# Optimization experiments

Hardware: AMD Instinct MI355X
Metric: run time of the kernel (lower is better)

Reference implementation:

```python
import jax, jax.numpy as jnp
import numpy as np

B, D, H = 64, 1024, 1024  # batch, input_dim, hidden_dim


def setup_inputs() -> dict:
    key = jax.random.key(0)
    k_x, k_inW, k_hW = jax.random.split(key, 3)
    # Observed binary inputs in {0,1} -> Bernoulli-sample branch never taken.
    x = jax.random.randint(k_x, (B, D), 0, 2).astype(jnp.float32)
    # Kaiming-normal init: std = sqrt(2 / fan_in)
    in_W = jax.random.normal(k_inW, (H, D), dtype=jnp.float32) * np.float32(np.sqrt(2.0 / D))
    in_b = jnp.zeros((H,), dtype=jnp.float32)
    h_W = jax.random.normal(k_hW, (D, H), dtype=jnp.float32) * np.float32(np.sqrt(2.0 / H))
    h_b = jnp.zeros((D,), dtype=jnp.float32)
    return {"x": x, "in_W": in_W, "in_b": in_b, "h_W": h_W, "h_b": h_b}


def reference(x, in_W, in_b, h_W, h_b):
    # NADE recurrence: a_i = in_b + sum_{j<i} x_j * in_W[:, j]
    # Vectorized via exclusive cumulative sum of rank-1 contributions.
    contrib = jnp.einsum("bd,hd->bdh", x, in_W)          # [B, D, H]
    cum = jnp.cumsum(contrib, axis=1)
    a = jnp.concatenate([jnp.zeros_like(cum[:, :1]), cum[:, :-1]], axis=1) + in_b  # exclusive
    h = jax.nn.relu(a)                                    # [B, D, H]
    # p_i = sigmoid(relu(a_i) . h_W[i] + h_b[i])
    p_hat = jax.nn.sigmoid(jnp.einsum("bdh,dh->bd", h, h_W) + h_b)  # [B, D]
    return p_hat
```

## Files before the change

### kernel.cpp

```cpp
#include <hip/hip_runtime.h>
#include <hip/hip_bf16.h>

#define B 64
#define D 1024
#define H 1024
#define C 32
#define L (D / C)

__device__ __forceinline__ float dpp_xor1(float v) {
    int i = __builtin_bit_cast(int, v);
    i = __builtin_amdgcn_mov_dpp(i, 0xB1, 0xF, 0xF, true);
    return __builtin_bit_cast(float, i);
}
__device__ __forceinline__ float dpp_xor2(float v) {
    int i = __builtin_bit_cast(int, v);
    i = __builtin_amdgcn_mov_dpp(i, 0x4E, 0xF, 0xF, true);
    return __builtin_bit_cast(float, i);
}

__global__ void k_transpose(const float* __restrict__ in, float* __restrict__ out) {
    __shared__ float tile[32][33];
    int bx = blockIdx.x * 32;
    int by = blockIdx.y * 32;
    int tx = threadIdx.x;
    int ty = threadIdx.y;
    #pragma unroll
    for (int r = 0; r < 32; r += 8)
        tile[ty + r][tx] = in[(by + ty + r) * D + (bx + tx)];
    __syncthreads();
    #pragma unroll
    for (int r = 0; r < 32; r += 8)
        out[(bx + ty + r) * H + (by + tx)] = tile[tx][ty + r];
}

__global__ void __launch_bounds__(256, 4)
k_chunk_sums(const float* __restrict__ x,
             const float* __restrict__ Wt,
             float* __restrict__ S) {
    int blk = blockIdx.x;
    int b = blk / C;
    int c = blk % C;
    int tid = threadIdx.x;
    int h0 = tid * 4;

    __shared__ unsigned mlds;
    float xv = (tid < L) ? x[b * D + c * L + tid] : 0.f;
    unsigned long long bal = __ballot(xv != 0.f);
    if (tid == 0) mlds = (unsigned)bal;
    __syncthreads();
    unsigned m = mlds;

    float4 acc = make_float4(0.f, 0.f, 0.f, 0.f);
    #pragma unroll
    for (int j = 0; j < L; ++j) {
        if (m & (1u << j)) {
            float4 w = *reinterpret_cast<const float4*>(&Wt[(size_t)(c * L + j) * H + h0]);
            acc.x += w.x; acc.y += w.y; acc.z += w.z; acc.w += w.w;
        }
    }
    *reinterpret_cast<float4*>(&S[((size_t)b * C + c) * H + h0]) = acc;
}

__global__ void k_scan(float* __restrict__ S) {
    int tid = blockIdx.x * blockDim.x + threadIdx.x;
    if (tid >= B * H) return;
    int b = tid / H;
    int h = tid % H;
    float run = 0.f;
    #pragma unroll
    for (int c = 0; c < C; ++c) {
        int idx = (b * C + c) * H + h;
        float v = S[idx];
        S[idx] = run;
        run += v;
    }
}

__global__ void __launch_bounds__(256, 4)
k_nade_main(const float* __restrict__ x,
            const float* __restrict__ Wt,
            const float* __restrict__ in_b,
            const float* __restrict__ h_W,
            const float* __restrict__ h_b,
            const float* __restrict__ P,
            float* __restrict__ out) {
    int blk = blockIdx.x;
    int b = blk / C;
    int c = blk % C;
    int tid = threadIdx.x;
    int h0 = tid * 4;
    int lane = tid & 63;
    int wv = tid >> 6;
    int ph = lane & 3;

    __shared__ unsigned mlds;
    float xv = (tid < L) ? x[b * D + c * L + tid] : 0.f;
    unsigned long long bal = __ballot(xv != 0.f);
    if (tid == 0) mlds = (unsigned)bal;

    float4 pv = *reinterpret_cast<const float4*>(&P[((size_t)b * C + c) * H + h0]);
    float4 ib = *reinterpret_cast<const float4*>(&in_b[h0]);
    float4 a;
    a.x = pv.x + ib.x; a.y = pv.y + ib.y; a.z = pv.z + ib.z; a.w = pv.w + ib.w;

    __syncthreads();
    unsigned m = mlds;

    float pr[8];
    #pragma unroll
    for (int s = 0; s < 8; ++s) pr[s] = 0.f;

    #pragma unroll
    for (int il = 0; il < L; ++il) {
        int i = c * L + il;
        float4 w = *reinterpret_cast<const float4*>(&h_W[(size_t)i * H + h0]);
        float p = fmaxf(a.x, 0.f) * w.x + fmaxf(a.y, 0.f) * w.y +
                  fmaxf(a.z, 0.f) * w.z + fmaxf(a.w, 0.f) * w.w;
        float t = p + dpp_xor1(p);
        t = t + dpp_xor2(t);
        pr[il >> 2] = (ph == (il & 3)) ? t : pr[il >> 2];

        if (m & (1u << il)) {
            float4 wv4 = *reinterpret_cast<const float4*>(&Wt[(size_t)i * H + h0]);
            a.x += wv4.x; a.y += wv4.y; a.z += wv4.z; a.w += wv4.w;
        }
    }

    #pragma unroll
    for (int s = 0; s < 8; ++s) {
        float v = pr[s];
        v += __shfl_xor(v, 4, 64);
        v += __shfl_xor(v, 8, 64);
        v += __shfl_xor(v, 16, 64);
        v += __shfl_xor(v, 32, 64);
        pr[s] = v;
    }

    __shared__ float red[4][L];
    if (lane < 4) {
        #pragma unroll
        for (int s = 0; s < 8; ++s)
            red[wv][s * 4 + lane] = pr[s];
    }
    __syncthreads();

    if (tid < L) {
        int i = c * L + tid;
        float t = red[0][tid] + red[1][tid] + red[2][tid] + red[3][tid] + h_b[i];
        out[(size_t)b * D + i] = 1.0f / (1.0f + expf(-t));
    }
}

extern "C" void kernel_launch(void* const* d_in, const int* in_sizes, int n_in,
                              void* d_out, int out_size, void* d_ws, size_t ws_size,
                              hipStream_t stream) {
    const float* x    = (const float*)d_in[0];
    const float* in_W = (const float*)d_in[1];
    const float* in_b = (const float*)d_in[2];
    const float* h_W  = (const float*)d_in[3];
    const float* h_b  = (const float*)d_in[4];
    float* out = (float*)d_out;

    float* Wt = (float*)d_ws;
    float* S  = Wt + (size_t)D * H;

    dim3 tb(32, 8);
    dim3 tg(D / 32, H / 32);
    k_transpose<<<tg, tb, 0, stream>>>(in_W, Wt);

    k_chunk_sums<<<B * C, 256, 0, stream>>>(x, Wt, S);

    k_scan<<<(B * H + 255) / 256, 256, 0, stream>>>(S);

    k_nade_main<<<B * C, 256, 0, stream>>>(x, Wt, in_b, h_W, h_b, S, out);
}
```

Before: 45.57 us.

## Batch four rows per block and split hidden dim into quarters with combine pass

Each block now handles four batch rows and a quarter of the hidden dimension, so each loaded weight element (Wt and h_W) is reused across four batch rows instead of one. The sparse bitmask skip of zero inputs is replaced by dense FMAs with x values staged in shared memory. Partial dot products per hidden quarter go to a new workspace buffer Q, and a new combine kernel sums them and applies the sigmoid. This cuts weight traffic by about 4x. The costs are an extra launch, extra global traffic for Q, more registers, and losing the skip over zero inputs.

```diff
diff --git a/kernel.cpp b/kernel.cpp
--- a/kernel.cpp
+++ b/kernel.cpp
@@ -6,6 +6,10 @@
 #define H 1024
 #define C 32
 #define L (D / C)
+#define BG 4
+#define NBG (B / BG)
+#define HQ 4
+#define HP (H / HQ)
 
 __device__ __forceinline__ float dpp_xor1(float v) {
     int i = __builtin_bit_cast(int, v);
@@ -33,32 +37,43 @@
         out[(bx + ty + r) * H + (by + tx)] = tile[tx][ty + r];
 }
 
-__global__ void __launch_bounds__(256, 4)
+__global__ void __launch_bounds__(256)
 k_chunk_sums(const float* __restrict__ x,
              const float* __restrict__ Wt,
              float* __restrict__ S) {
     int blk = blockIdx.x;
-    int b = blk / C;
-    int c = blk % C;
+    int bg  = blk >> 7;
+    int chq = blk & 127;
+    int c   = chq >> 2;
+    int hq  = chq & 3;
+    int b0  = bg * BG;
     int tid = threadIdx.x;
-    int h0 = tid * 4;
-
-    __shared__ unsigned mlds;
-    float xv = (tid < L) ? x[b * D + c * L + tid] : 0.f;
-    unsigned long long bal = __ballot(xv != 0.f);
-    if (tid == 0) mlds = (unsigned)bal;
-    __syncthreads();
-    unsigned m = mlds;
-
-    float4 acc = make_float4(0.f, 0.f, 0.f, 0.f);
+    int h   = hq * HP + tid;
+
+    __shared__ float4 xs4[L];
+    if (tid < L) {
+        int i = c * L + tid;
+        xs4[tid] = make_float4(x[(size_t)b0 * D + i],
+                               x[(size_t)(b0 + 1) * D + i],
+                               x[(size_t)(b0 + 2) * D + i],
+                               x[(size_t)(b0 + 3) * D + i]);
+    }
+    __syncthreads();
+
+    float acc0 = 0.f, acc1 = 0.f, acc2 = 0.f, acc3 = 0.f;
     #pragma unroll
     for (int j = 0; j < L; ++j) {
-        if (m & (1u << j)) {
-            float4 w = *reinterpret_cast<const float4*>(&Wt[(size_t)(c * L + j) * H + h0]);
-            acc.x += w.x; acc.y += w.y; acc.z += w.z; acc.w += w.w;
-        }
-    }
-    *reinterpret_cast<float4*>(&S[((size_t)b * C + c) * H + h0]) = acc;
+        float w = Wt[(size_t)(c * L + j) * H + h];
+        float4 xf = xs4[j];
+        acc0 = fmaf(xf.x, w, acc0);
+        acc1 = fmaf(xf.y, w, acc1);
+        acc2 = fmaf(xf.z, w, acc2);
+        acc3 = fmaf(xf.w, w, acc3);
+    }
+    S[((size_t)b0 * C + c) * H + h]       = acc0;
+    S[((size_t)(b0 + 1) * C + c) * H + h] = acc1;
+    S[((size_t)(b0 + 2) * C + c) * H + h] = acc2;
+    S[((size_t)(b0 + 3) * C + c) * H + h] = acc3;
 }
 
 __global__ void k_scan(float* __restrict__ S) {
@@ -76,79 +91,130 @@
     }
 }
 
-__global__ void __launch_bounds__(256, 4)
+__global__ void __launch_bounds__(256)
 k_nade_main(const float* __restrict__ x,
             const float* __restrict__ Wt,
             const float* __restrict__ in_b,
             const float* __restrict__ h_W,
             const float* __restrict__ h_b,
             const float* __restrict__ P,
-            float* __restrict__ out) {
+            float* __restrict__ Q) {
     int blk = blockIdx.x;
-    int b = blk / C;
-    int c = blk % C;
+    int bg  = blk >> 7;
+    int chq = blk & 127;
+    int c   = chq >> 2;
+    int hq  = chq & 3;
+    int b0  = bg * BG;
     int tid = threadIdx.x;
-    int h0 = tid * 4;
+    int h   = hq * HP + tid;
     int lane = tid & 63;
     int wv = tid >> 6;
     int ph = lane & 3;
 
-    __shared__ unsigned mlds;
-    float xv = (tid < L) ? x[b * D + c * L + tid] : 0.f;
-    unsigned long long bal = __ballot(xv != 0.f);
-    if (tid == 0) mlds = (unsigned)bal;
-
-    float4 pv = *reinterpret_cast<const float4*>(&P[((size_t)b * C + c) * H + h0]);
-    float4 ib = *reinterpret_cast<const float4*>(&in_b[h0]);
-    float4 a;
-    a.x = pv.x + ib.x; a.y = pv.y + ib.y; a.z = pv.z + ib.z; a.w = pv.w + ib.w;
-
-    __syncthreads();
-    unsigned m = mlds;
-
-    float pr[8];
-    #pragma unroll
-    for (int s = 0; s < 8; ++s) pr[s] = 0.f;
+    __shared__ float4 xs4[L];
+    if (tid < L) {
+        int i = c * L + tid;
+        xs4[tid] = make_float4(x[(size_t)b0 * D + i],
+                               x[(size_t)(b0 + 1) * D + i],
+                               x[(size_t)(b0 + 2) * D + i],
+                               x[(size_t)(b0 + 3) * D + i]);
+    }
+
+    float ib = in_b[h];
+    float a0 = P[((size_t)b0 * C + c) * H + h] + ib;
+    float a1 = P[((size_t)(b0 + 1) * C + c) * H + h] + ib;
+    float a2 = P[((size_t)(b0 + 2) * C + c) * H + h] + ib;
+    float a3 = P[((size_t)(b0 + 3) * C + c) * H + h] + ib;
+
+    __syncthreads();
+
+    bool k0 = (ph == 0), k1 = (ph == 1), k2 = (ph == 2), k3 = (ph == 3);
+
+    float pr0[8], pr1[8], pr2[8], pr3[8];
+    #pragma unroll
+    for (int s = 0; s < 8; ++s) { pr0[s] = 0.f; pr1[s] = 0.f; pr2[s] = 0.f; pr3[s] = 0.f; }
 
     #pragma unroll
     for (int il = 0; il < L; ++il) {
         int i = c * L + il;
-        float4 w = *reinterpret_cast<const float4*>(&h_W[(size_t)i * H + h0]);
-        float p = fmaxf(a.x, 0.f) * w.x + fmaxf(a.y, 0.f) * w.y +
-                  fmaxf(a.z, 0.f) * w.z + fmaxf(a.w, 0.f) * w.w;
-        float t = p + dpp_xor1(p);
-        t = t + dpp_xor2(t);
-        pr[il >> 2] = (ph == (il & 3)) ? t : pr[il >> 2];
-
-        if (m & (1u << il)) {
-            float4 wv4 = *reinterpret_cast<const float4*>(&Wt[(size_t)i * H + h0]);
-            a.x += wv4.x; a.y += wv4.y; a.z += wv4.z; a.w += wv4.w;
-        }
+        float w  = h_W[(size_t)i * H + h];
+        float wt = Wt[(size_t)i * H + h];
+        float4 xf = xs4[il];
+        int s = il >> 2;
+        bool keep = (il & 3) == 0 ? k0 : ((il & 3) == 1 ? k1 : ((il & 3) == 2 ? k2 : k3));
+
+        float p0 = fmaxf(a0, 0.f) * w;
+        float t0 = p0 + dpp_xor1(p0); t0 = t0 + dpp_xor2(t0);
+        pr0[s] = keep ? t0 : pr0[s];
+        a0 = fmaf(xf.x, wt, a0);
+
+        float p1 = fmaxf(a1, 0.f) * w;
+        float t1 = p1 + dpp_xor1(p1); t1 = t1 + dpp_xor2(t1);
+        pr1[s] = keep ? t1 : pr1[s];
+        a1 = fmaf(xf.y, wt, a1);
+
+        float p2 = fmaxf(a2, 0.f) * w;
+        float t2 = p2 + dpp_xor1(p2); t2 = t2 + dpp_xor2(t2);
+        pr2[s] = keep ? t2 : pr2[s];
+        a2 = fmaf(xf.z, wt, a2);
+
+        float p3 = fmaxf(a3, 0.f) * w;
+        float t3 = p3 + dpp_xor1(p3); t3 = t3 + dpp_xor2(t3);
+        pr3[s] = keep ? t3 : pr3[s];
+        a3 = fmaf(xf.w, wt, a3);
     }
 
     #pragma unroll
     for (int s = 0; s < 8; ++s) {
-        float v = pr[s];
-        v += __shfl_xor(v, 4, 64);
-        v += __shfl_xor(v, 8, 64);
-        v += __shfl_xor(v, 16, 64);
-        v += __shfl_xor(v, 32, 64);
-        pr[s] = v;
-    }
-
-    __shared__ float red[4][L];
+        float v;
+        v = pr0[s];
+        v += __shfl_xor(v, 4, 64); v += __shfl_xor(v, 8, 64);
+        v += __shfl_xor(v, 16, 64); v += __shfl_xor(v, 32, 64);
+        pr0[s] = v;
+        v = pr1[s];
+        v += __shfl_xor(v, 4, 64); v += __shfl_xor(v, 8, 64);
+        v += __shfl_xor(v, 16, 64); v += __shfl_xor(v, 32, 64);
+        pr1[s] = v;
+        v = pr2[s];
+        v += __shfl_xor(v, 4, 64); v += __shfl_xor(v, 8, 64);
+        v += __shfl_xor(v, 16, 64); v += __shfl_xor(v, 32, 64);
+        pr2[s] = v;
+        v = pr3[s];
+        v += __shfl_xor(v, 4, 64); v += __shfl_xor(v, 8, 64);
+        v += __shfl_xor(v, 16, 64); v += __shfl_xor(v, 32, 64);
+        pr3[s] = v;
+    }
+
+    __shared__ float red[4][BG][L];
     if (lane < 4) {
         #pragma unroll
-        for (int s = 0; s < 8; ++s)
-            red[wv][s * 4 + lane] = pr[s];
-    }
-    __syncthreads();
-
-    if (tid < L) {
-        int i = c * L + tid;
-        float t = red[0][tid] + red[1][tid] + red[2][tid] + red[3][tid] + h_b[i];
-        out[(size_t)b * D + i] = 1.0f / (1.0f + expf(-t));
-    }
+        for (int s = 0; s < 8; ++s) {
+            red[wv][0][s * 4 + lane] = pr0[s];
+            red[wv][1][s * 4 + lane] = pr1[s];
+            red[wv][2][s * 4 + lane] = pr2[s];
+            red[wv][3][s * 4 + lane] = pr3[s];
+        }
+    }
+    __syncthreads();
+
+    if (tid < BG * L) {
+        int b = tid >> 5;
+        int il = tid & 31;
+        float t = red[0][b][il] + red[1][b][il] + red[2][b][il] + red[3][b][il];
+        Q[((size_t)hq * B + (b0 + b)) * D + c * L + il] = t;
+    }
+}
+
+__global__ void __launch_bounds__(256)
+k_combine(const float* __restrict__ Q,
+          const float* __restrict__ h_b,
+          float* __restrict__ out) {
+    int idx = blockIdx.x * blockDim.x + threadIdx.x;
+    if (idx >= B * D) return;
+    int d = idx & (D - 1);
+    float t = Q[idx] + Q[(size_t)B * D + idx] + Q[2 * (size_t)B * D + idx]
+            + Q[3 * (size_t)B * D + idx] + h_b[d];
+    out[idx] = 1.0f / (1.0f + expf(-t));
 }
 
 extern "C" void kernel_launch(void* const* d_in, const int* in_sizes, int n_in,
@@ -163,14 +229,17 @@
 
     float* Wt = (float*)d_ws;
     float* S  = Wt + (size_t)D * H;
+    float* Q  = S + (size_t)B * C * H;
 
     dim3 tb(32, 8);
     dim3 tg(D / 32, H / 32);
     k_transpose<<<tg, tb, 0, stream>>>(in_W, Wt);
 
-    k_chunk_sums<<<B * C, 256, 0, stream>>>(x, Wt, S);
+    k_chunk_sums<<<NBG * C * HQ, 256, 0, stream>>>(x, Wt, S);
 
     k_scan<<<(B * H + 255) / 256, 256, 0, stream>>>(S);
 
-    k_nade_main<<<B * C, 256, 0, stream>>>(x, Wt, in_b, h_W, h_b, S, out);
-}
+    k_nade_main<<<NBG * C * HQ, 256, 0, stream>>>(x, Wt, in_b, h_W, h_b, S, Q);
+
+    k_combine<<<(B * D + 255) / 256, 256, 0, stream>>>(Q, h_b, out);
+}
```

Result: faster. 41.20 us (-9.6%).
